# Kernel tuning notes

Hardware: AMD Instinct MI355X
Metric: run time of the kernel (lower is better)

Reference implementation:

```python
import jax, jax.numpy as jnp
import numpy as np

F = 256          # number of features (input_size)
H1, H2, H3 = 128, 64, 32
OUT = 1          # output_size


def setup_inputs() -> dict:
    key = jax.random.key(0)
    ks = jax.random.split(key, 10)
    B = 8192
    # Kaiming-uniform-ish small init; exact init doesn't matter for a math reference.
    def w(k, shape, fan_in):
        lim = 1.0 / np.sqrt(fan_in)
        return jax.random.uniform(k, shape, jnp.float32, -lim, lim)
    return {
        "x": jax.random.normal(ks[0], (B, F), dtype=jnp.float32),
        "W1": w(ks[1], (F, H1), 1),          # Linear(1 -> H1) per feature
        "b1": w(ks[2], (F, H1), 1),
        "W2": w(ks[3], (F, H1, H2), H1),
        "b2": w(ks[4], (F, H2), H1),
        "W3": w(ks[5], (F, H2, H3), H2),
        "b3": w(ks[6], (F, H3), H2),
        "W4": w(ks[7], (F, H3, OUT), H3),
        "b4": w(ks[8], (F, OUT), H3),
        "bias": jnp.zeros((OUT,), dtype=jnp.float32),
    }


def reference(x, W1, b1, W2, b2, W3, b3, W4, b4, bias):
    # Fused form of the per-feature FeatureNN loop (eval mode: dropout = identity).
    # Layer 1: scalar input per feature -> H1
    h = jax.nn.relu(x[:, :, None] * W1[None, :, :] + b1[None, :, :])   # [B,F,H1]
    h = jax.nn.relu(jnp.einsum('bfh,fhk->bfk', h, W2) + b2[None])      # [B,F,H2]
    h = jax.nn.relu(jnp.einsum('bfh,fhk->bfk', h, W3) + b3[None])      # [B,F,H3]
    f_out = jnp.einsum('bfh,fhk->bfk', h, W4) + b4[None]               # [B,F,OUT]
    # torch.cat(dim=1).sum(dim=1, keepdim=True): sum over features and output cols
    out = jnp.sum(f_out, axis=(1, 2), keepdims=False)[:, None] + bias[None, :]
    return out  # [B, OUT] with OUT==1
```

## Files before the change

kernel.cpp:

```cpp
#include <hip/hip_runtime.h>
#include <math.h>


#define NF   256
#define NH1  128
#define NH2  64
#define NH3  32
#define NB   8192

#define NRANK 129
#define ROW4  17
#define ROWH  136
#define TBLDW 8960
#define XT_DW (NF * TBLDW)

typedef float    f32x16 __attribute__((ext_vector_type(16)));
typedef unsigned u32x4  __attribute__((ext_vector_type(4)));
typedef _Float16 h16x2  __attribute__((ext_vector_type(2)));
typedef _Float16 h16x8  __attribute__((ext_vector_type(8)));

__device__ __forceinline__ unsigned pkh2(unsigned sw, unsigned sb, h16x2 xh) {
    h16x2 r = __builtin_elementwise_fma(xh, __builtin_bit_cast(h16x2, sw),
                                            __builtin_bit_cast(h16x2, sb));
    h16x2 hz = {(_Float16)0.f, (_Float16)0.f};
    return __builtin_bit_cast(unsigned, __builtin_elementwise_max(r, hz));
}

__global__ __launch_bounds__(1024) void build_tables(
    const float* __restrict__ x,
    const float* __restrict__ W1, const float* __restrict__ b1,
    const float* __restrict__ W2, const float* __restrict__ b2,
    const float* __restrict__ bias, float* __restrict__ out,
    unsigned* __restrict__ ws)
{
    __shared__ u32x4 SP4[NRANK * ROW4];
    __shared__ float rkey[NH1];
    __shared__ float skey[NH1];
    __shared__ int   sidx[NH1];
    __shared__ float w1s[NH1], b1s[NH1];
    __shared__ float Pbw[16][NH2], Pbb[16][NH2], Pdw[16][NH2], Pdb[16][NH2];
    __shared__ float xtile[64][65];

    const int f = blockIdx.x;
    const int t = (int)threadIdx.x;
    _Float16* SPh = (_Float16*)SP4;

    const int gid = f * 1024 + t;
    if (gid < NB) out[gid] = bias[0];

    const float* __restrict__ gw2 = W2 + (size_t)f * NH1 * NH2;
    if (t < NH1) {
        float w  = W1[f * NH1 + t];
        float bb = b1[f * NH1 + t];
        w1s[t] = w; b1s[t] = bb;
        rkey[t] = (w != 0.0f) ? (-bb / w) : INFINITY;
    }
    __syncthreads();

    if (t < NH1) {
        const float my = rkey[t];
        int rk = 0;
        #pragma unroll 16
        for (int i = 0; i < NH1; ++i) {
            float ki = rkey[i];
            rk += (ki < my || (ki == my && i < t)) ? 1 : 0;
        }
        skey[rk] = my; sidx[rk] = t;
    }
    __syncthreads();

    {
        const int k = t & 63, c = t >> 6;
        float bw = 0.0f, bbp = 0.0f, dw = 0.0f, db = 0.0f;
        #pragma unroll
        for (int i = 0; i < 8; ++i) {
            int j = c * 8 + i;
            float w = w1s[j], bv = b1s[j], w2v = gw2[j * NH2 + k];
            if (w < 0.0f) { bw = fmaf(w, w2v, bw); bbp = fmaf(bv, w2v, bbp); }
            else if (w == 0.0f && bv > 0.0f) { bbp = fmaf(bv, w2v, bbp); }
            int jj = sidx[c * 8 + i];
            float ww = w1s[jj], bv2 = b1s[jj], w2x = gw2[jj * NH2 + k];
            float s = (ww > 0.0f) ? 1.0f : ((ww < 0.0f) ? -1.0f : 0.0f);
            dw = fmaf(s * ww,  w2x, dw);
            db = fmaf(s * bv2, w2x, db);
        }
        Pbw[c][k] = bw; Pbb[c][k] = bbp; Pdw[c][k] = dw; Pdb[c][k] = db;
    }
    __syncthreads();
    {
        const int k = t & 63, c = t >> 6;
        float accw = 0.0f;
        float accb = b2[f * NH2 + k];
        #pragma unroll
        for (int c2 = 0; c2 < 16; ++c2) { accw += Pbw[c2][k]; accb += Pbb[c2][k]; }
        for (int c2 = 0; c2 < c; ++c2) { accw += Pdw[c2][k]; accb += Pdb[c2][k]; }
        if (c == 0) {
            SPh[k]      = (_Float16)accw;
            SPh[64 + k] = (_Float16)accb;
        }
        #pragma unroll
        for (int i = 0; i < 8; ++i) {
            int r = c * 8 + i;
            int j = sidx[r];
            float w = w1s[j], bv = b1s[j], w2v = gw2[j * NH2 + k];
            float s = (w > 0.0f) ? 1.0f : ((w < 0.0f) ? -1.0f : 0.0f);
            accw = fmaf(s * w,  w2v, accw);
            accb = fmaf(s * bv, w2v, accb);
            SPh[(r + 1) * ROWH + k]      = (_Float16)accw;
            SPh[(r + 1) * ROWH + 64 + k] = (_Float16)accb;
        }
    }
    __syncthreads();

    unsigned* __restrict__ wsf = ws + (size_t)f * TBLDW;
    if (t < NH1) wsf[t] = __float_as_uint(skey[t]);
    const u32x4* src = (const u32x4*)SP4;
    u32x4* dst = (u32x4*)(wsf + NH1);
    for (int i = t; i < NRANK * ROW4; i += 1024) dst[i] = src[i];

    float* __restrict__ xt = (float*)(ws + XT_DW);
    #pragma unroll 1
    for (int tt = 0; tt < 2; ++tt) {
        const int T  = f * 2 + tt;
        const int bt = T >> 2, ft = T & 3;
        __syncthreads();
        #pragma unroll
        for (int it = 0; it < 4; ++it) {
            int idx = t + it * 1024;
            int rr = idx >> 6, cc = idx & 63;
            xtile[rr][cc] = x[(size_t)(bt * 64 + rr) * NF + ft * 64 + cc];
        }
        __syncthreads();
        #pragma unroll
        for (int it = 0; it < 4; ++it) {
            int idx = t + it * 1024;
            int cc = idx >> 6, rr = idx & 63;
            xt[(size_t)(ft * 64 + cc) * NB + bt * 64 + rr] = xtile[rr][cc];
        }
    }
}

__global__ __launch_bounds__(512, 4) void nam_main(
    const float* __restrict__ W3, const float* __restrict__ b3,
    const float* __restrict__ W4, const float* __restrict__ b4,
    const unsigned* __restrict__ ws,
    float* __restrict__ out)
{
    __shared__ u32x4 SP4[NRANK * ROW4];
    __shared__ float tkey[NH1];

    const int f  = blockIdx.x >> 2;
    const int qt = blockIdx.x & 3;
    const int t  = (int)threadIdx.x;

    const unsigned* __restrict__ wsf = ws + (size_t)f * TBLDW;
    if (t < NH1) tkey[t] = __uint_as_float(wsf[t]);
    {
        const u32x4* src = (const u32x4*)(wsf + NH1);
        #pragma unroll 2
        for (int i = t; i < NRANK * ROW4; i += 512) SP4[i] = src[i];
    }
    __syncthreads();

    const int lane = t & 63, wv = t >> 6;
    const int n = lane & 31, q2 = lane >> 5;

    const float* __restrict__ w3g = W3 + f * NH2 * NH3;
    h16x8 A0, A1, A2, A3;
    #pragma unroll
    for (int j = 0; j < 8; ++j) {
        int kk = q2 * 8 + j;
        A0[j] = (_Float16)w3g[kk * NH3 + n];
        A1[j] = (_Float16)w3g[(kk + 16) * NH3 + n];
        A2[j] = (_Float16)w3g[(kk + 32) * NH3 + n];
        A3[j] = (_Float16)w3g[(kk + 48) * NH3 + n];
    }
    f32x16 bacc;
    float w4r[16];
    #pragma unroll
    for (int reg = 0; reg < 16; ++reg) {
        int row = (reg & 3) + 8 * (reg >> 2) + 4 * q2;
        bacc[reg] = b3[f * NH3 + row];
        w4r[reg]  = W4[f * NH3 + row];
    }
    const float b4f = b4[f];
    const float* __restrict__ xrow = (const float*)(ws + XT_DW) + (size_t)f * NB;
    const float t63 = tkey[63], t31 = tkey[31], t95 = tkey[95];
    const float t15 = tkey[15], t47 = tkey[47], t79 = tkey[79], t111 = tkey[111];

    auto rankof = [&](float q) -> int {
        int rr = (t63 < q) ? 64 : 0;
        {
            float l1 = (rr & 64) ? t95 : t31;
            if (l1 < q) rr += 32;
            float m0 = (rr & 64) ? t79  : t15;
            float m1 = (rr & 64) ? t111 : t47;
            float l2 = (rr & 32) ? m1 : m0;
            if (l2 < q) rr += 16;
        }
        #pragma unroll
        for (int s = 8; s > 0; s >>= 1)
            if (tkey[rr + s - 1] < q) rr += s;
        return rr;
    };

    const int base0 = qt * 2048 + wv * 32;
    float xv = xrow[base0 + n];
    int r = rankof(xv);

    #pragma unroll 1
    for (int round = 0; round < 8; ++round) {
        const int base = base0 + round * 256;

        const float xnext = xrow[(base + 256 + n) & (NB - 1)];

        const int ro = r * ROW4;
        u32x4 SW0 = SP4[ro + q2],      SW1 = SP4[ro + 2 + q2];
        u32x4 SW2 = SP4[ro + 4 + q2],  SW3 = SP4[ro + 6 + q2];
        u32x4 SB0 = SP4[ro + 8 + q2],  SB1 = SP4[ro + 10 + q2];
        u32x4 SB2 = SP4[ro + 12 + q2], SB3 = SP4[ro + 14 + q2];

        const h16x2 xh = {(_Float16)xv, (_Float16)xv};
        u32x4 d0, d1, d2, d3;
        d0.x = pkh2(SW0.x, SB0.x, xh); d0.y = pkh2(SW0.y, SB0.y, xh);
        d0.z = pkh2(SW0.z, SB0.z, xh); d0.w = pkh2(SW0.w, SB0.w, xh);
        d1.x = pkh2(SW1.x, SB1.x, xh); d1.y = pkh2(SW1.y, SB1.y, xh);
        d1.z = pkh2(SW1.z, SB1.z, xh); d1.w = pkh2(SW1.w, SB1.w, xh);
        d2.x = pkh2(SW2.x, SB2.x, xh); d2.y = pkh2(SW2.y, SB2.y, xh);
        d2.z = pkh2(SW2.z, SB2.z, xh); d2.w = pkh2(SW2.w, SB2.w, xh);
        d3.x = pkh2(SW3.x, SB3.x, xh); d3.y = pkh2(SW3.y, SB3.y, xh);
        d3.z = pkh2(SW3.z, SB3.z, xh); d3.w = pkh2(SW3.w, SB3.w, xh);
        h16x8 B0 = __builtin_bit_cast(h16x8, d0);
        h16x8 B1 = __builtin_bit_cast(h16x8, d1);
        h16x8 B2 = __builtin_bit_cast(h16x8, d2);
        h16x8 B3 = __builtin_bit_cast(h16x8, d3);

        f32x16 acc = __builtin_amdgcn_mfma_f32_32x32x16_f16(A0, B0, bacc, 0, 0, 0);
        acc = __builtin_amdgcn_mfma_f32_32x32x16_f16(A1, B1, acc, 0, 0, 0);
        acc = __builtin_amdgcn_mfma_f32_32x32x16_f16(A2, B2, acc, 0, 0, 0);
        acc = __builtin_amdgcn_mfma_f32_32x32x16_f16(A3, B3, acc, 0, 0, 0);

        const int rnext = rankof(xnext);

        float p = 0.0f;
        #pragma unroll
        for (int reg = 0; reg < 16; ++reg)
            p = fmaf(fmaxf(acc[reg], 0.0f), w4r[reg], p);
        p += __shfl_xor(p, 32);
        if (lane < 32) atomicAdd(&out[base + lane], p + b4f);

        xv = xnext; r = rnext;
    }
}

extern "C" void kernel_launch(void* const* d_in, const int* in_sizes, int n_in,
                              void* d_out, int out_size, void* d_ws, size_t ws_size,
                              hipStream_t stream) {
    const float* x    = (const float*)d_in[0];
    const float* W1   = (const float*)d_in[1];
    const float* b1   = (const float*)d_in[2];
    const float* W2   = (const float*)d_in[3];
    const float* b2   = (const float*)d_in[4];
    const float* W3   = (const float*)d_in[5];
    const float* b3   = (const float*)d_in[6];
    const float* W4   = (const float*)d_in[7];
    const float* b4   = (const float*)d_in[8];
    const float* bias = (const float*)d_in[9];
    float* out   = (float*)d_out;
    unsigned* ws = (unsigned*)d_ws;

    build_tables<<<NF, 1024, 0, stream>>>(x, W1, b1, W2, b2, bias, out, ws);
    nam_main<<<NF * 4, 512, 0, stream>>>(W3, b3, W4, b4, ws, out);
}
```

Before: 120.1 us.

## Fuse table build into main kernel and split x transpose into separate kernel

The piecewise-linear table construction now happens in the same block that consumes it, so the table never round-trips through global workspace. The x transpose moves to its own 512-block kernel. The main kernel drops from 1024 blocks of 512 threads to 256 blocks of 1024 threads, each covering all 8192 batch rows for one feature, with the batch chunk order staggered by feature. In exchange there are fewer, larger blocks and less parallelism for the sorted-key search and matmul phase, and the table build is repeated per block instead of shared across four blocks.

```diff
diff --git a/kernel.cpp b/kernel.cpp
--- a/kernel.cpp
+++ b/kernel.cpp
@@ -11,8 +11,6 @@
 #define NRANK 129
 #define ROW4  17
 #define ROWH  136
-#define TBLDW 8960
-#define XT_DW (NF * TBLDW)
 
 typedef float    f32x16 __attribute__((ext_vector_type(16)));
 typedef unsigned u32x4  __attribute__((ext_vector_type(4)));
@@ -26,12 +24,39 @@
     return __builtin_bit_cast(unsigned, __builtin_elementwise_max(r, hz));
 }
 
-__global__ __launch_bounds__(1024) void build_tables(
-    const float* __restrict__ x,
+__global__ __launch_bounds__(1024) void transpose_x(
+    const float* __restrict__ x, const float* __restrict__ bias,
+    float* __restrict__ out, float* __restrict__ xt)
+{
+    __shared__ float xtile[64][65];
+    const int t = (int)threadIdx.x;
+    const int T = blockIdx.x;
+    const int bt = T >> 2, ft = T & 3;
+
+    if (T < 8) out[T * 1024 + t] = bias[0];
+
+    #pragma unroll
+    for (int it = 0; it < 4; ++it) {
+        int idx = t + it * 1024;
+        int rr = idx >> 6, cc = idx & 63;
+        xtile[rr][cc] = x[(size_t)(bt * 64 + rr) * NF + ft * 64 + cc];
+    }
+    __syncthreads();
+    #pragma unroll
+    for (int it = 0; it < 4; ++it) {
+        int idx = t + it * 1024;
+        int cc = idx >> 6, rr = idx & 63;
+        xt[(size_t)(ft * 64 + cc) * NB + bt * 64 + rr] = xtile[rr][cc];
+    }
+}
+
+__global__ __launch_bounds__(1024) void nam_fused(
     const float* __restrict__ W1, const float* __restrict__ b1,
     const float* __restrict__ W2, const float* __restrict__ b2,
-    const float* __restrict__ bias, float* __restrict__ out,
-    unsigned* __restrict__ ws)
+    const float* __restrict__ W3, const float* __restrict__ b3,
+    const float* __restrict__ W4, const float* __restrict__ b4,
+    const float* __restrict__ xt,
+    float* __restrict__ out)
 {
     __shared__ u32x4 SP4[NRANK * ROW4];
     __shared__ float rkey[NH1];
@@ -39,14 +64,10 @@
     __shared__ int   sidx[NH1];
     __shared__ float w1s[NH1], b1s[NH1];
     __shared__ float Pbw[16][NH2], Pbb[16][NH2], Pdw[16][NH2], Pdb[16][NH2];
-    __shared__ float xtile[64][65];
 
     const int f = blockIdx.x;
     const int t = (int)threadIdx.x;
     _Float16* SPh = (_Float16*)SP4;
-
-    const int gid = f * 1024 + t;
-    if (gid < NB) out[gid] = bias[0];
 
     const float* __restrict__ gw2 = W2 + (size_t)f * NH1 * NH2;
     if (t < NH1) {
@@ -112,56 +133,6 @@
     }
     __syncthreads();
 
-    unsigned* __restrict__ wsf = ws + (size_t)f * TBLDW;
-    if (t < NH1) wsf[t] = __float_as_uint(skey[t]);
-    const u32x4* src = (const u32x4*)SP4;
-    u32x4* dst = (u32x4*)(wsf + NH1);
-    for (int i = t; i < NRANK * ROW4; i += 1024) dst[i] = src[i];
-
-    float* __restrict__ xt = (float*)(ws + XT_DW);
-    #pragma unroll 1
-    for (int tt = 0; tt < 2; ++tt) {
-        const int T  = f * 2 + tt;
-        const int bt = T >> 2, ft = T & 3;
-        __syncthreads();
-        #pragma unroll
-        for (int it = 0; it < 4; ++it) {
-            int idx = t + it * 1024;
-            int rr = idx >> 6, cc = idx & 63;
-            xtile[rr][cc] = x[(size_t)(bt * 64 + rr) * NF + ft * 64 + cc];
-        }
-        __syncthreads();
-        #pragma unroll
-        for (int it = 0; it < 4; ++it) {
-            int idx = t + it * 1024;
-            int cc = idx >> 6, rr = idx & 63;
-            xt[(size_t)(ft * 64 + cc) * NB + bt * 64 + rr] = xtile[rr][cc];
-        }
-    }
-}
-
-__global__ __launch_bounds__(512, 4) void nam_main(
-    const float* __restrict__ W3, const float* __restrict__ b3,
-    const float* __restrict__ W4, const float* __restrict__ b4,
-    const unsigned* __restrict__ ws,
-    float* __restrict__ out)
-{
-    __shared__ u32x4 SP4[NRANK * ROW4];
-    __shared__ float tkey[NH1];
-
-    const int f  = blockIdx.x >> 2;
-    const int qt = blockIdx.x & 3;
-    const int t  = (int)threadIdx.x;
-
-    const unsigned* __restrict__ wsf = ws + (size_t)f * TBLDW;
-    if (t < NH1) tkey[t] = __uint_as_float(wsf[t]);
-    {
-        const u32x4* src = (const u32x4*)(wsf + NH1);
-        #pragma unroll 2
-        for (int i = t; i < NRANK * ROW4; i += 512) SP4[i] = src[i];
-    }
-    __syncthreads();
-
     const int lane = t & 63, wv = t >> 6;
     const int n = lane & 31, q2 = lane >> 5;
 
@@ -184,9 +155,9 @@
         w4r[reg]  = W4[f * NH3 + row];
     }
     const float b4f = b4[f];
-    const float* __restrict__ xrow = (const float*)(ws + XT_DW) + (size_t)f * NB;
-    const float t63 = tkey[63], t31 = tkey[31], t95 = tkey[95];
-    const float t15 = tkey[15], t47 = tkey[47], t79 = tkey[79], t111 = tkey[111];
+    const float* __restrict__ xrow = xt + (size_t)f * NB;
+    const float t63 = skey[63], t31 = skey[31], t95 = skey[95];
+    const float t15 = skey[15], t47 = skey[47], t79 = skey[79], t111 = skey[111];
 
     auto rankof = [&](float q) -> int {
         int rr = (t63 < q) ? 64 : 0;
@@ -200,19 +171,18 @@
         }
         #pragma unroll
         for (int s = 8; s > 0; s >>= 1)
-            if (tkey[rr + s - 1] < q) rr += s;
+            if (skey[rr + s - 1] < q) rr += s;
         return rr;
     };
 
-    const int base0 = qt * 2048 + wv * 32;
-    float xv = xrow[base0 + n];
+    const int boff = wv * 32 + n;
+    float xv = xrow[((0 + f) & 15) * 512 + boff];
     int r = rankof(xv);
 
     #pragma unroll 1
-    for (int round = 0; round < 8; ++round) {
-        const int base = base0 + round * 256;
-
-        const float xnext = xrow[(base + 256 + n) & (NB - 1)];
+    for (int round = 0; round < 16; ++round) {
+        const int base = (((round + f) & 15) * 16 + wv) * 32;
+        const float xnext = xrow[(((round + 1 + f) & 15) * 16 + wv) * 32 + n];
 
         const int ro = r * ROW4;
         u32x4 SW0 = SP4[ro + q2],      SW1 = SP4[ro + 2 + q2];
@@ -267,8 +237,8 @@
     const float* b4   = (const float*)d_in[8];
     const float* bias = (const float*)d_in[9];
     float* out   = (float*)d_out;
-    unsigned* ws = (unsigned*)d_ws;
-
-    build_tables<<<NF, 1024, 0, stream>>>(x, W1, b1, W2, b2, bias, out, ws);
-    nam_main<<<NF * 4, 512, 0, stream>>>(W3, b3, W4, b4, ws, out);
-}
+    float* xtw   = (float*)d_ws;
+
+    transpose_x<<<512, 1024, 0, stream>>>(x, bias, out, xtw);
+    nam_fused<<<NF, 1024, 0, stream>>>(W1, b1, W2, b2, W3, b3, W4, b4, xtw, out);
+}
```

Measured after the change: 111.7 us. -7.0%, faster.
